# Kernel optimization log

Measured on AMD Instinct MI355X. Metric: run time of the kernel, lower is better.

## Reference

```python
import jax, jax.numpy as jnp
import numpy as np

B, C, H, W = 2, 256, 64, 64
NUM_HEADS = 4
HEAD_DIM = C // NUM_HEADS
N = H * W


def setup_inputs() -> dict:
    key = jax.random.key(0)
    ks = jax.random.split(key, 10)
    x = jax.random.normal(ks[0], (B, C, H, W), dtype=jnp.float32)
    # mostly-True mask; diagonal forced True so every row has a valid key
    m = jax.random.uniform(ks[1], (B, N, N)) > 0.1
    spatial_mask = m | jnp.eye(N, dtype=bool)[None]
    s = 1.0 / np.sqrt(C)
    wq = jax.random.normal(ks[2], (C, C), dtype=jnp.float32) * s
    bq = jnp.zeros((C,), jnp.float32)
    wk = jax.random.normal(ks[3], (C, C), dtype=jnp.float32) * s
    bk = jnp.zeros((C,), jnp.float32)
    wv = jax.random.normal(ks[4], (C, C), dtype=jnp.float32) * s
    bv = jnp.zeros((C,), jnp.float32)
    # torch zero-inits out_proj; use random weights for a non-trivial baseline
    wo = jax.random.normal(ks[5], (C, C), dtype=jnp.float32) * s
    bo = jnp.zeros((C,), jnp.float32)
    return {"x": x, "spatial_mask": spatial_mask, "wq": wq, "bq": bq,
            "wk": wk, "bk": bk, "wv": wv, "bv": bv, "wo": wo, "bo": bo}


def reference(x, spatial_mask, wq, bq, wk, bk, wv, bv, wo, bo):
    b, c, h, w = x.shape
    n = h * w
    nh, hd = NUM_HEADS, HEAD_DIM
    scale = hd ** -0.5
    x_flat = x.reshape(b, c, n).transpose(0, 2, 1)           # [b, n, c]
    q = (x_flat @ wq.T + bq).reshape(b, n, nh, hd).transpose(0, 2, 1, 3)
    k = (x_flat @ wk.T + bk).reshape(b, n, nh, hd).transpose(0, 2, 1, 3)
    v = (x_flat @ wv.T + bv).reshape(b, n, nh, hd).transpose(0, 2, 1, 3)
    logits = jnp.einsum('bhqd,bhkd->bhqk', q, k) * scale      # [b, nh, n, n]
    logits = jnp.where(spatial_mask[:, None], logits, -jnp.inf)
    attn = jax.nn.softmax(logits, axis=-1)                    # dropout = identity (eval)
    out = jnp.einsum('bhqk,bhkd->bhqd', attn, v)              # [b, nh, n, hd]
    out = out.transpose(0, 2, 1, 3).reshape(b, n, c)
    out = out @ wo.T + bo
    return out.transpose(0, 2, 1).reshape(b, c, h, w)
```

## Files before the change

### kernel.cpp

```cpp
#include <hip/hip_runtime.h>
#include <math.h>

namespace {
constexpr int B_    = 2;
constexpr int C_    = 256;
constexpr int NHEAD = 4;
constexpr int HDIM  = 64;
constexpr int NTOK  = 4096;
constexpr float SCALE = 0.125f;
constexpr float LOG2E = 1.44269504f;
}

typedef _Float16 half8  __attribute__((ext_vector_type(8)));
typedef _Float16 half4  __attribute__((ext_vector_type(4)));
typedef __fp16   fp16x2 __attribute__((ext_vector_type(2)));
typedef float    floatx4 __attribute__((ext_vector_type(4)));
typedef int      int4v   __attribute__((ext_vector_type(4)));
typedef unsigned int uint2v __attribute__((ext_vector_type(2)));

__device__ __forceinline__ void plswap32(int &a, int &b) {
#if __has_builtin(__builtin_amdgcn_permlane32_swap)
    const uint2v r = __builtin_amdgcn_permlane32_swap((unsigned)a, (unsigned)b, false, false);
    a = (int)r[0]; b = (int)r[1];
#else
    asm volatile("s_nop 1\n\tv_permlane32_swap_b32 %0, %1\n\ts_nop 1"
                 : "+v"(a), "+v"(b));
#endif
}
__device__ __forceinline__ void plswap16(int &a, int &b) {
#if __has_builtin(__builtin_amdgcn_permlane16_swap)
    const uint2v r = __builtin_amdgcn_permlane16_swap((unsigned)a, (unsigned)b, false, false);
    a = (int)r[0]; b = (int)r[1];
#else
    asm volatile("s_nop 1\n\tv_permlane16_swap_b32 %0, %1\n\ts_nop 1"
                 : "+v"(a), "+v"(b));
#endif
}

__global__ __launch_bounds__(256) void pack_mask(
    const unsigned int* __restrict__ m32, unsigned int* __restrict__ packed)
{
    int c0 = 0, c1 = 0, c2 = 0, c3 = 0;
    #pragma unroll
    for (int i = 0; i < 16; i++) {
        const unsigned int d = m32[i];
        c0 += (d == 0x00000001u);
        c1 += (d == 0x3F803F80u);
        c2 += (d == 0x3F800000u);
        c3 += (d == 0x01010101u);
    }
    int fmt = 1, best = c1;
    if (c0 > best) { best = c0; fmt = 0; }
    if (c2 > best) { best = c2; fmt = 2; }
    if (c3 > best) { best = c3; fmt = 3; }

    const unsigned int W = blockIdx.x * 256 + threadIdx.x;
    unsigned int bits = 0;
    if (fmt == 1) {
        const uint4* p4 = (const uint4*)(m32 + (size_t)W * 16);
        #pragma unroll
        for (int i = 0; i < 4; i++) {
            const uint4 v = p4[i];
            const unsigned int d[4] = { v.x, v.y, v.z, v.w };
            #pragma unroll
            for (int j = 0; j < 4; j++) {
                const int e = i * 8 + j * 2;
                bits |= ((d[j] & 0xFFFFu) ? 1u : 0u) << e;
                bits |= ((d[j] >> 16)     ? 1u : 0u) << (e + 1);
            }
        }
    } else if (fmt != 3) {
        const uint4* p4 = (const uint4*)(m32 + (size_t)W * 32);
        #pragma unroll
        for (int i = 0; i < 8; i++) {
            const uint4 v = p4[i];
            bits |= (v.x ? 1u : 0u) << (i * 4 + 0);
            bits |= (v.y ? 1u : 0u) << (i * 4 + 1);
            bits |= (v.z ? 1u : 0u) << (i * 4 + 2);
            bits |= (v.w ? 1u : 0u) << (i * 4 + 3);
        }
    } else {
        const uint4* p4 = (const uint4*)(m32 + (size_t)W * 8);
        #pragma unroll
        for (int i = 0; i < 2; i++) {
            const uint4 v = p4[i];
            const unsigned int d[4] = { v.x, v.y, v.z, v.w };
            #pragma unroll
            for (int j = 0; j < 4; j++) {
                const int e = (i * 4 + j) * 4;
                bits |= ((d[j] & 0x000000FFu) ? 1u : 0u) << (e + 0);
                bits |= ((d[j] & 0x0000FF00u) ? 1u : 0u) << (e + 1);
                bits |= ((d[j] & 0x00FF0000u) ? 1u : 0u) << (e + 2);
                bits |= ((d[j] & 0xFF000000u) ? 1u : 0u) << (e + 3);
            }
        }
    }
    packed[W] = bits;
}

__global__ __launch_bounds__(256) void qkv_mfma(
    const float* __restrict__ x,
    const float* __restrict__ wq, const float* __restrict__ bq,
    const float* __restrict__ wk, const float* __restrict__ bk,
    const float* __restrict__ wv, const float* __restrict__ bv,
    _Float16* __restrict__ qo, _Float16* __restrict__ ko,
    _Float16* __restrict__ vo)
{
    const int nt = blockIdx.x;
    const int b  = blockIdx.y;
    const int p  = blockIdx.z;

    const float* w; const float* bias;
    if (p == 0)      { w = wq; bias = bq; }
    else if (p == 1) { w = wk; bias = bk; }
    else             { w = wv; bias = bv; }

    const int t    = threadIdx.x;
    const int wid  = t >> 6;
    const int lane = t & 63;
    const int quad = lane >> 4;
    const int l15  = lane & 15;
    const int n0   = nt * 64;

    __shared__ _Float16 xsh[64 * 264];
    __shared__ _Float16 wsh[64 * 72];
    __shared__ _Float16 tbuf[64 * 72];

    const int srow = t >> 2;
    const int sc   = (t & 3) * 16;

    {
        const int cr = t >> 4;
        const int nu = (t & 15) * 4;
        const float* xb = x + (size_t)b * C_ * NTOK;
        #pragma unroll
        for (int cc = 0; cc < 16; cc++) {
            const int cl = cc * 16 + cr;
            const float4 v = *(const float4*)&xb[(size_t)cl * NTOK + n0 + nu];
            xsh[(nu + 0) * 264 + cl] = (_Float16)v.x;
            xsh[(nu + 1) * 264 + cl] = (_Float16)v.y;
            xsh[(nu + 2) * 264 + cl] = (_Float16)v.z;
            xsh[(nu + 3) * 264 + cl] = (_Float16)v.w;
        }
    }

    for (int h = 0; h < NHEAD; h++) {
        const int co0 = h * 64;
        floatx4 acc[4];
        #pragma unroll
        for (int i = 0; i < 4; i++) acc[i] = (floatx4)0.f;

        for (int c0 = 0; c0 < C_; c0 += 64) {
            {
                const float* wr = &w[(size_t)(co0 + srow) * C_ + c0 + sc];
                half8 h0, h1;
                #pragma unroll
                for (int u = 0; u < 2; u++) {
                    const float4 a = *(const float4*)&wr[u * 4];
                    h0[u*4+0]=(_Float16)a.x; h0[u*4+1]=(_Float16)a.y;
                    h0[u*4+2]=(_Float16)a.z; h0[u*4+3]=(_Float16)a.w;
                }
                #pragma unroll
                for (int u = 0; u < 2; u++) {
                    const float4 a = *(const float4*)&wr[8 + u * 4];
                    h1[u*4+0]=(_Float16)a.x; h1[u*4+1]=(_Float16)a.y;
                    h1[u*4+2]=(_Float16)a.z; h1[u*4+3]=(_Float16)a.w;
                }
                *(half8*)&wsh[srow * 72 + sc]     = h0;
                *(half8*)&wsh[srow * 72 + sc + 8] = h1;
            }
            __syncthreads();
            const half8 a0 = *(const half8*)&wsh[(wid * 16 + l15) * 72 + quad * 8];
            const half8 a1 = *(const half8*)&wsh[(wid * 16 + l15) * 72 + 32 + quad * 8];
            #pragma unroll
            for (int nt2 = 0; nt2 < 4; nt2++) {
                const half8 b0 = *(const half8*)&xsh[(nt2 * 16 + l15) * 264 + c0 + quad * 8];
                const half8 b1 = *(const half8*)&xsh[(nt2 * 16 + l15) * 264 + c0 + 32 + quad * 8];
                acc[nt2] = __builtin_amdgcn_mfma_f32_16x16x32_f16(a0, b0, acc[nt2], 0, 0, 0);
                acc[nt2] = __builtin_amdgcn_mfma_f32_16x16x32_f16(a1, b1, acc[nt2], 0, 0, 0);
            }
            __syncthreads();
        }

        const float4 bb4 = *(const float4*)&bias[co0 + wid * 16 + quad * 4];
        const float bb[4] = { bb4.x, bb4.y, bb4.z, bb4.w };

        if (p < 2) {
            const float osc = (p == 0) ? (SCALE * LOG2E) : 1.0f;
            #pragma unroll
            for (int nt2 = 0; nt2 < 4; nt2++) {
                half4 hv;
                #pragma unroll
                for (int i = 0; i < 4; i++)
                    hv[i] = (_Float16)((acc[nt2][i] + bb[i]) * osc);
                *(half4*)&tbuf[(nt2 * 16 + l15) * 72 + wid * 16 + quad * 4] = hv;
            }
            __syncthreads();
            _Float16* dh = (p == 0 ? qo : ko) + (size_t)(b * NHEAD + h) * NTOK * HDIM;
            const half8 o0 = *(const half8*)&tbuf[srow * 72 + sc];
            const half8 o1 = *(const half8*)&tbuf[srow * 72 + sc + 8];
            *(half8*)&dh[(size_t)(n0 + srow) * HDIM + sc]     = o0;
            *(half8*)&dh[(size_t)(n0 + srow) * HDIM + sc + 8] = o1;
        } else {
            #pragma unroll
            for (int nt2 = 0; nt2 < 4; nt2++)
                #pragma unroll
                for (int i = 0; i < 4; i++)
                    tbuf[(wid * 16 + quad * 4 + i) * 72 + nt2 * 16 + l15] =
                        (_Float16)(acc[nt2][i] + bb[i]);
            __syncthreads();
            _Float16* vth = vo + (size_t)(b * NHEAD + h) * HDIM * NTOK;
            const half8 o0 = *(const half8*)&tbuf[srow * 72 + sc];
            const half8 o1 = *(const half8*)&tbuf[srow * 72 + sc + 8];
            *(half8*)&vth[(size_t)srow * NTOK + n0 + sc]     = o0;
            *(half8*)&vth[(size_t)srow * NTOK + n0 + sc + 8] = o1;
        }
        __syncthreads();
    }
}

__global__ __launch_bounds__(512) void attn(
    const _Float16* __restrict__ q, const _Float16* __restrict__ k,
    const _Float16* __restrict__ vt, const unsigned int* __restrict__ mpacked,
    _Float16* __restrict__ ao)
{
    const int b  = blockIdx.z;
    const int h  = blockIdx.y;
    const int q0 = blockIdx.x * 64;
    const int t    = threadIdx.x;
    const int w    = t >> 6;
    const int lane = t & 63;
    const int quad = lane >> 4;
    const int l15  = lane & 15;
    const int half = w >> 2;
    const int w4   = w & 3;
    const int koff = half * (NTOK / 2);

    __shared__ __align__(16) char smem_raw[2 * 4 * 64 * 72 * 2];
    _Float16* const sbase = (_Float16*)(smem_raw + half * 36864);

    const size_t head_off = (size_t)(b * NHEAD + h) * NTOK * HDIM;
    const _Float16* qb  = q  + head_off;
    const _Float16* kb  = k  + head_off;
    const _Float16* vtb = vt + head_off;
    const unsigned int* mrow = mpacked + (size_t)b * NTOK * 128;

    const int qrow = q0 + w4 * 16 + l15;
    half8 aq0 = *(const half8*)&qb[(size_t)qrow * HDIM + quad * 8];
    half8 aq1 = *(const half8*)&qb[(size_t)qrow * HDIM + 32 + quad * 8];
    const unsigned int* mq = &mrow[(size_t)qrow * 128];

    const int tl   = t & 255;
    const int srow = tl >> 2;
    const int scol = (tl & 3) * 16;

    half8 kreg0 = *(const half8*)&kb[(size_t)(koff + srow) * HDIM + scol];
    half8 kreg1 = *(const half8*)&kb[(size_t)(koff + srow) * HDIM + scol + 8];
    half8 vreg0 = *(const half8*)&vtb[(size_t)srow * NTOK + koff + scol];
    half8 vreg1 = *(const half8*)&vtb[(size_t)srow * NTOK + koff + scol + 8];

    uint2 mw = *(const uint2*)&mq[koff >> 5];
    uint2 mw_nxt = mw;

    float l_loc = 0.f;
    floatx4 o_acc[4];
    #pragma unroll
    for (int i = 0; i < 4; i++) o_acc[i] = (floatx4)0.f;

    *(half8*)&sbase[srow * 72 + scol]            = kreg0;
    *(half8*)&sbase[srow * 72 + scol + 8]        = kreg1;
    *(half8*)&sbase[4608 + srow * 72 + scol]     = vreg0;
    *(half8*)&sbase[4608 + srow * 72 + scol + 8] = vreg1;
    __syncthreads();

#define SOFTMAX_CT(CT, WORD, SH, Pa, Pb)                                          \
    {                                                                             \
        const unsigned nib = ((WORD) >> ((SH) + quad * 4)) & 0xFu;                \
        const float p0 = __builtin_amdgcn_exp2f((nib & 1u) ? sa[CT][0] : -3.0e38f);\
        const float p1 = __builtin_amdgcn_exp2f((nib & 2u) ? sa[CT][1] : -3.0e38f);\
        const float p2 = __builtin_amdgcn_exp2f((nib & 4u) ? sa[CT][2] : -3.0e38f);\
        const float p3 = __builtin_amdgcn_exp2f((nib & 8u) ? sa[CT][3] : -3.0e38f);\
        l_loc += (p0 + p1) + (p2 + p3);                                           \
        Pa = __builtin_bit_cast(int, __builtin_amdgcn_cvt_pkrtz(p0, p1));         \
        Pb = __builtin_bit_cast(int, __builtin_amdgcn_cvt_pkrtz(p2, p3));         \
    }

#define ATTN_TILE(RO, WO, KT, PF)                                                 \
    {                                                                             \
        if (PF) {                                                                 \
            const int k0n = koff + (KT) * 64 + 64;                                \
            kreg0 = *(const half8*)&kb[(size_t)(k0n + srow) * HDIM + scol];       \
            kreg1 = *(const half8*)&kb[(size_t)(k0n + srow) * HDIM + scol + 8];   \
            vreg0 = *(const half8*)&vtb[(size_t)srow * NTOK + k0n + scol];        \
            vreg1 = *(const half8*)&vtb[(size_t)srow * NTOK + k0n + scol + 8];    \
            mw_nxt = *(const uint2*)&mq[k0n >> 5];                                \
        }                                                                         \
        floatx4 sa[4];                                                            \
        __builtin_amdgcn_s_setprio(1);                                            \
        _Pragma("unroll")                                                         \
        for (int ct = 0; ct < 4; ct++) {                                          \
            sa[ct] = (floatx4)0.f;                                                \
            const half8 ka0 = *(const half8*)&sbase[(RO) + (ct*16 + l15)*72 + quad*8];      \
            const half8 ka1 = *(const half8*)&sbase[(RO) + (ct*16 + l15)*72 + 32 + quad*8]; \
            sa[ct] = __builtin_amdgcn_mfma_f32_16x16x32_f16(ka0, aq0, sa[ct], 0, 0, 0);     \
            sa[ct] = __builtin_amdgcn_mfma_f32_16x16x32_f16(ka1, aq1, sa[ct], 0, 0, 0);     \
        }                                                                         \
        __builtin_amdgcn_s_setprio(0);                                            \
        int P00, P01, P10, P11, P20, P21, P30, P31;                               \
        SOFTMAX_CT(0, mw.x, 0,  P00, P01)                                         \
        SOFTMAX_CT(1, mw.x, 16, P10, P11)                                         \
        SOFTMAX_CT(2, mw.y, 0,  P20, P21)                                         \
        SOFTMAX_CT(3, mw.y, 16, P30, P31)                                         \
        mw = mw_nxt;                                                              \
                                                   \
        plswap32(P00, P10); plswap32(P01, P11);                                   \
        plswap32(P20, P30); plswap32(P21, P31);                                   \
                                               \
        plswap16(P00, P10); plswap16(P01, P11);                                   \
        plswap16(P20, P30); plswap16(P21, P31);                                   \
        const half8 pb0 = __builtin_bit_cast(half8, (int4v){P00, P01, P10, P11}); \
        const half8 pb1 = __builtin_bit_cast(half8, (int4v){P20, P21, P30, P31}); \
        __builtin_amdgcn_s_setprio(1);                                            \
        _Pragma("unroll")                                                         \
        for (int dt = 0; dt < 4; dt++) {                                          \
            const half8 va0 = *(const half8*)&sbase[(RO) + 4608 + (dt*16 + l15)*72 + quad*8];      \
            const half8 va1 = *(const half8*)&sbase[(RO) + 4608 + (dt*16 + l15)*72 + 32 + quad*8]; \
            o_acc[dt] = __builtin_amdgcn_mfma_f32_16x16x32_f16(va0, pb0, o_acc[dt], 0, 0, 0);      \
            o_acc[dt] = __builtin_amdgcn_mfma_f32_16x16x32_f16(va1, pb1, o_acc[dt], 0, 0, 0);      \
        }                                                                         \
        __builtin_amdgcn_s_setprio(0);                                            \
        if (PF) {                                                                 \
            *(half8*)&sbase[(WO) + srow * 72 + scol]            = kreg0;          \
            *(half8*)&sbase[(WO) + srow * 72 + scol + 8]        = kreg1;          \
            *(half8*)&sbase[(WO) + 4608 + srow * 72 + scol]     = vreg0;          \
            *(half8*)&sbase[(WO) + 4608 + srow * 72 + scol + 8] = vreg1;          \
        }                                                                         \
        __syncthreads();                                                          \
    }

    for (int kt2 = 0; kt2 < 15; kt2++) {
        ATTN_TILE(0,    9216, 2 * kt2,     1)
        ATTN_TILE(9216, 0,    2 * kt2 + 1, 1)
    }
    ATTN_TILE(0,    9216, 30, 1)
    ATTN_TILE(9216, 0,    31, 0)

#undef ATTN_TILE
#undef SOFTMAX_CT

    l_loc += __shfl_xor(l_loc, 16, 64);
    l_loc += __shfl_xor(l_loc, 32, 64);

    float* oex = (float*)smem_raw;
    float* lex = (float*)(smem_raw + 16384);
    if (w >= 4) {
        float* dst = &oex[((size_t)(w - 4) * 64 + lane) * 16];
        #pragma unroll
        for (int dt = 0; dt < 4; dt++)
            *(floatx4*)&dst[dt * 4] = o_acc[dt];
        if (quad == 0) lex[(w - 4) * 16 + l15] = l_loc;
    }
    __syncthreads();
    if (w < 4) {
        const float* src = &oex[((size_t)w * 64 + lane) * 16];
        const float lt = l_loc + lex[w * 16 + l15];
        const float inv = (lt > 0.f) ? (1.0f / lt) : 0.f;
        _Float16* aob = ao + ((size_t)b * NTOK + q0 + w * 16 + l15) * C_ + h * 64;
        #pragma unroll
        for (int dt = 0; dt < 4; dt++) {
            const floatx4 o2 = *(const floatx4*)&src[dt * 4];
            half4 r;
            #pragma unroll
            for (int rr = 0; rr < 4; rr++)
                r[rr] = (_Float16)((o_acc[dt][rr] + o2[rr]) * inv);
            *(half4*)&aob[dt * 16 + quad * 4] = r;
        }
    }
}

__global__ __launch_bounds__(256) void out_mfma(
    const _Float16* __restrict__ ao, const float* __restrict__ wo,
    const float* __restrict__ bo, float* __restrict__ out)
{
    const int nt  = blockIdx.x;
    const int cot = blockIdx.y;
    const int b   = blockIdx.z;
    const int t    = threadIdx.x;
    const int wid  = t >> 6;
    const int lane = t & 63;
    const int quad = lane >> 4;
    const int l15  = lane & 15;
    const int n0  = nt * 64;
    const int co0 = cot * 64;

    __shared__ _Float16 wsh[64 * 72];
    __shared__ _Float16 ash[64 * 72];
    __shared__ float    tf[64 * 68];

    const int srow = t >> 2;
    const int sc   = (t & 3) * 16;

    floatx4 acc[4];
    #pragma unroll
    for (int i = 0; i < 4; i++) acc[i] = (floatx4)0.f;

    const _Float16* aob = ao + ((size_t)b * NTOK + n0) * C_;

    for (int c0 = 0; c0 < C_; c0 += 64) {
        {
            const float* wr = &wo[(size_t)(co0 + srow) * C_ + c0 + sc];
            half8 h0, h1;
            #pragma unroll
            for (int u = 0; u < 2; u++) {
                const float4 a = *(const float4*)&wr[u * 4];
                h0[u*4+0]=(_Float16)a.x; h0[u*4+1]=(_Float16)a.y;
                h0[u*4+2]=(_Float16)a.z; h0[u*4+3]=(_Float16)a.w;
            }
            #pragma unroll
            for (int u = 0; u < 2; u++) {
                const float4 a = *(const float4*)&wr[8 + u * 4];
                h1[u*4+0]=(_Float16)a.x; h1[u*4+1]=(_Float16)a.y;
                h1[u*4+2]=(_Float16)a.z; h1[u*4+3]=(_Float16)a.w;
            }
            *(half8*)&wsh[srow * 72 + sc]     = h0;
            *(half8*)&wsh[srow * 72 + sc + 8] = h1;
        }
        {
            const _Float16* ar = &aob[(size_t)srow * C_ + c0 + sc];
            *(half8*)&ash[srow * 72 + sc]     = *(const half8*)&ar[0];
            *(half8*)&ash[srow * 72 + sc + 8] = *(const half8*)&ar[8];
        }
        __syncthreads();
        const half8 a0 = *(const half8*)&wsh[(wid * 16 + l15) * 72 + quad * 8];
        const half8 a1 = *(const half8*)&wsh[(wid * 16 + l15) * 72 + 32 + quad * 8];
        #pragma unroll
        for (int nt2 = 0; nt2 < 4; nt2++) {
            const half8 b0 = *(const half8*)&ash[(nt2 * 16 + l15) * 72 + quad * 8];
            const half8 b1 = *(const half8*)&ash[(nt2 * 16 + l15) * 72 + 32 + quad * 8];
            acc[nt2] = __builtin_amdgcn_mfma_f32_16x16x32_f16(a0, b0, acc[nt2], 0, 0, 0);
            acc[nt2] = __builtin_amdgcn_mfma_f32_16x16x32_f16(a1, b1, acc[nt2], 0, 0, 0);
        }
        __syncthreads();
    }

    #pragma unroll
    for (int nt2 = 0; nt2 < 4; nt2++)
        #pragma unroll
        for (int i = 0; i < 4; i++)
            tf[(wid * 16 + quad * 4 + i) * 68 + nt2 * 16 + l15] = acc[nt2][i];
    __syncthreads();

    const int row = t >> 2;
    const int c4  = (t & 3) * 16;
    const float bb = bo[co0 + row];
    float* orow = &out[((size_t)(b * C_ + co0 + row)) * NTOK + n0 + c4];
    #pragma unroll
    for (int u = 0; u < 4; u++) {
        float4 v = *(const float4*)&tf[row * 68 + c4 + u * 4];
        v.x += bb; v.y += bb; v.z += bb; v.w += bb;
        *(float4*)&orow[u * 4] = v;
    }
}

extern "C" void kernel_launch(void* const* d_in, const int* in_sizes, int n_in,
                              void* d_out, int out_size, void* d_ws, size_t ws_size,
                              hipStream_t stream) {
    const float* x    = (const float*)d_in[0];
    const void*  mask = d_in[1];
    const float* wq   = (const float*)d_in[2];
    const float* bq   = (const float*)d_in[3];
    const float* wk   = (const float*)d_in[4];
    const float* bk   = (const float*)d_in[5];
    const float* wv   = (const float*)d_in[6];
    const float* bv   = (const float*)d_in[7];
    const float* wo   = (const float*)d_in[8];
    const float* bo   = (const float*)d_in[9];
    float* out = (float*)d_out;

    const size_t qkv_elems = (size_t)B_ * NHEAD * NTOK * HDIM;
    _Float16* wsh = (_Float16*)d_ws;
    _Float16* qbuf  = wsh;
    _Float16* kbuf  = wsh + qkv_elems;
    _Float16* vtbuf = wsh + 2 * qkv_elems;
    _Float16* aobuf = wsh + 3 * qkv_elems;
    unsigned int* mpacked = (unsigned int*)(wsh + 4 * qkv_elems);

    pack_mask<<<dim3((B_ * NTOK * 128) / 256), 256, 0, stream>>>(
        (const unsigned int*)mask, mpacked);
    qkv_mfma<<<dim3(NTOK / 64, B_, 3), 256, 0, stream>>>(
        x, wq, bq, wk, bk, wv, bv, qbuf, kbuf, vtbuf);
    attn<<<dim3(NTOK / 64, NHEAD, B_), 512, 0, stream>>>(
        qbuf, kbuf, vtbuf, mpacked, aobuf);
    out_mfma<<<dim3(NTOK / 64, C_ / 64, B_), 256, 0, stream>>>(
        aobuf, wo, bo, out);
}
```

Measured before the change: 298.6 us.

## Stage K/V tiles via direct global-to-LDS loads with XOR-swizzled layout

Replaces the register-staged K and V prefetch (global load to VGPRs, then a store to LDS after compute) with global_load_lds direct transfers into shared memory. The padded 72-stride layout is replaced by an unpadded 64-stride layout with an XOR swizzle to avoid bank conflicts. This is meant to remove VGPR pressure and the explicit LDS store instructions. The risk is that the asynchronous writes into the other buffer may race without explicit vmcnt waits, and the swizzle may fail to remove conflicts on reads.

```diff
diff --git a/kernel.cpp b/kernel.cpp
--- a/kernel.cpp
+++ b/kernel.cpp
@@ -34,6 +34,16 @@
 #else
     asm volatile("s_nop 1\n\tv_permlane16_swap_b32 %0, %1\n\ts_nop 1"
                  : "+v"(a), "+v"(b));
+#endif
+}
+
+__device__ __forceinline__ void gload_lds16(const _Float16* g, _Float16* l, int lane) {
+#if __has_builtin(__builtin_amdgcn_global_load_lds)
+    __builtin_amdgcn_global_load_lds(
+        (const __attribute__((address_space(1))) void*)g,
+        (__attribute__((address_space(3))) void*)l, 16, 0, 0);
+#else
+    *(half8*)((char*)l + lane * 16) = *(const half8*)g;
 #endif
 }
 
@@ -236,8 +246,8 @@
     const int w4   = w & 3;
     const int koff = half * (NTOK / 2);
 
-    __shared__ __align__(16) char smem_raw[2 * 4 * 64 * 72 * 2];
-    _Float16* const sbase = (_Float16*)(smem_raw + half * 36864);
+    __shared__ __align__(16) char smem_raw[65536];
+    _Float16* const sbase = (_Float16*)(smem_raw + half * 32768);
 
     const size_t head_off = (size_t)(b * NHEAD + h) * NTOK * HDIM;
     const _Float16* qb  = q  + head_off;
@@ -250,14 +260,9 @@
     half8 aq1 = *(const half8*)&qb[(size_t)qrow * HDIM + 32 + quad * 8];
     const unsigned int* mq = &mrow[(size_t)qrow * 128];
 
-    const int tl   = t & 255;
-    const int srow = tl >> 2;
-    const int scol = (tl & 3) * 16;
-
-    half8 kreg0 = *(const half8*)&kb[(size_t)(koff + srow) * HDIM + scol];
-    half8 kreg1 = *(const half8*)&kb[(size_t)(koff + srow) * HDIM + scol + 8];
-    half8 vreg0 = *(const half8*)&vtb[(size_t)srow * NTOK + koff + scol];
-    half8 vreg1 = *(const half8*)&vtb[(size_t)srow * NTOK + koff + scol + 8];
+    const int jr  = l15 & 7;
+    const int xs0 = (quad ^ jr) << 3;
+    const int xs1 = ((quad + 4) ^ jr) << 3;
 
     uint2 mw = *(const uint2*)&mq[koff >> 5];
     uint2 mw_nxt = mw;
@@ -267,10 +272,22 @@
     #pragma unroll
     for (int i = 0; i < 4; i++) o_acc[i] = (floatx4)0.f;
 
-    *(half8*)&sbase[srow * 72 + scol]            = kreg0;
-    *(half8*)&sbase[srow * 72 + scol + 8]        = kreg1;
-    *(half8*)&sbase[4608 + srow * 72 + scol]     = vreg0;
-    *(half8*)&sbase[4608 + srow * 72 + scol + 8] = vreg1;
+#define STAGE(WO, K0N)                                                        \
+    {                                                                         \
+        const int rl = lane >> 3;                       \
+        const int xc = ((lane & 7) ^ rl) << 3;        \
+        const int c0 = w4 * 2, c1 = c0 + 1;                                   \
+        gload_lds16(&kb[(size_t)((K0N) + c0 * 8 + rl) * HDIM + xc],           \
+                    &sbase[(WO) + c0 * 512], lane);                           \
+        gload_lds16(&kb[(size_t)((K0N) + c1 * 8 + rl) * HDIM + xc],           \
+                    &sbase[(WO) + c1 * 512], lane);                           \
+        gload_lds16(&vtb[(size_t)(c0 * 8 + rl) * NTOK + (K0N) + xc],          \
+                    &sbase[(WO) + 4096 + c0 * 512], lane);                    \
+        gload_lds16(&vtb[(size_t)(c1 * 8 + rl) * NTOK + (K0N) + xc],          \
+                    &sbase[(WO) + 4096 + c1 * 512], lane);                    \
+    }
+
+    STAGE(0, koff)
     __syncthreads();
 
 #define SOFTMAX_CT(CT, WORD, SH, Pa, Pb)                                          \
@@ -289,10 +306,7 @@
     {                                                                             \
         if (PF) {                                                                 \
             const int k0n = koff + (KT) * 64 + 64;                                \
-            kreg0 = *(const half8*)&kb[(size_t)(k0n + srow) * HDIM + scol];       \
-            kreg1 = *(const half8*)&kb[(size_t)(k0n + srow) * HDIM + scol + 8];   \
-            vreg0 = *(const half8*)&vtb[(size_t)srow * NTOK + k0n + scol];        \
-            vreg1 = *(const half8*)&vtb[(size_t)srow * NTOK + k0n + scol + 8];    \
+            STAGE(WO, k0n)                                                        \
             mw_nxt = *(const uint2*)&mq[k0n >> 5];                                \
         }                                                                         \
         floatx4 sa[4];                                                            \
@@ -300,8 +314,8 @@
         _Pragma("unroll")                                                         \
         for (int ct = 0; ct < 4; ct++) {                                          \
             sa[ct] = (floatx4)0.f;                                                \
-            const half8 ka0 = *(const half8*)&sbase[(RO) + (ct*16 + l15)*72 + quad*8];      \
-            const half8 ka1 = *(const half8*)&sbase[(RO) + (ct*16 + l15)*72 + 32 + quad*8]; \
+            const half8 ka0 = *(const half8*)&sbase[(RO) + (ct*16 + l15)*64 + xs0];\
+            const half8 ka1 = *(const half8*)&sbase[(RO) + (ct*16 + l15)*64 + xs1];\
             sa[ct] = __builtin_amdgcn_mfma_f32_16x16x32_f16(ka0, aq0, sa[ct], 0, 0, 0);     \
             sa[ct] = __builtin_amdgcn_mfma_f32_16x16x32_f16(ka1, aq1, sa[ct], 0, 0, 0);     \
         }                                                                         \
@@ -323,30 +337,25 @@
         __builtin_amdgcn_s_setprio(1);                                            \
         _Pragma("unroll")                                                         \
         for (int dt = 0; dt < 4; dt++) {                                          \
-            const half8 va0 = *(const half8*)&sbase[(RO) + 4608 + (dt*16 + l15)*72 + quad*8];      \
-            const half8 va1 = *(const half8*)&sbase[(RO) + 4608 + (dt*16 + l15)*72 + 32 + quad*8]; \
+            const half8 va0 = *(const half8*)&sbase[(RO) + 4096 + (dt*16 + l15)*64 + xs0];\
+            const half8 va1 = *(const half8*)&sbase[(RO) + 4096 + (dt*16 + l15)*64 + xs1];\
             o_acc[dt] = __builtin_amdgcn_mfma_f32_16x16x32_f16(va0, pb0, o_acc[dt], 0, 0, 0);      \
             o_acc[dt] = __builtin_amdgcn_mfma_f32_16x16x32_f16(va1, pb1, o_acc[dt], 0, 0, 0);      \
         }                                                                         \
         __builtin_amdgcn_s_setprio(0);                                            \
-        if (PF) {                                                                 \
-            *(half8*)&sbase[(WO) + srow * 72 + scol]            = kreg0;          \
-            *(half8*)&sbase[(WO) + srow * 72 + scol + 8]        = kreg1;          \
-            *(half8*)&sbase[(WO) + 4608 + srow * 72 + scol]     = vreg0;          \
-            *(half8*)&sbase[(WO) + 4608 + srow * 72 + scol + 8] = vreg1;          \
-        }                                                                         \
         __syncthreads();                                                          \
     }
 
     for (int kt2 = 0; kt2 < 15; kt2++) {
-        ATTN_TILE(0,    9216, 2 * kt2,     1)
-        ATTN_TILE(9216, 0,    2 * kt2 + 1, 1)
-    }
-    ATTN_TILE(0,    9216, 30, 1)
-    ATTN_TILE(9216, 0,    31, 0)
+        ATTN_TILE(0,    8192, 2 * kt2,     1)
+        ATTN_TILE(8192, 0,    2 * kt2 + 1, 1)
+    }
+    ATTN_TILE(0,    8192, 30, 1)
+    ATTN_TILE(8192, 0,    31, 0)
 
 #undef ATTN_TILE
 #undef SOFTMAX_CT
+#undef STAGE
 
     l_loc += __shfl_xor(l_loc, 16, 64);
     l_loc += __shfl_xor(l_loc, 32, 64);
```

Measured after the change: 296.4 us. About the same (-0.7%).
